# Performance work log

Measured on AMD Instinct MI355X. Metric: run time of the kernel, lower is better.

The kernel has to match this reference:

```python
import jax, jax.numpy as jnp
import numpy as np

B, S, D, H = 2, 2048, 1024, 16
HD = D // H  # 64
ROPE_BASE = 10000.0


def setup_inputs() -> dict:
    key = jax.random.key(0)
    k1, k2, k3 = jax.random.split(key, 3)
    std = 1.0 / np.sqrt(D)
    x = jax.random.normal(k1, (B, S, D), dtype=jnp.float32)
    w_in = jax.random.normal(k2, (3 * D, D), dtype=jnp.float32) * std
    w_out = jax.random.normal(k3, (D, D), dtype=jnp.float32) * (std / np.sqrt(2.0))
    return {"x": x, "w_in": w_in, "w_out": w_out}


def _rope_cos_sin(seq_len, head_dim):
    inv_freq = 1.0 / (ROPE_BASE ** (jnp.arange(0, head_dim, 2, dtype=jnp.float32) / head_dim))
    t = jnp.arange(seq_len, dtype=jnp.float32)
    freqs = jnp.einsum("s,d->sd", t, inv_freq)          # [S, HD/2]
    emb = jnp.concatenate([freqs, freqs], axis=-1)       # [S, HD]
    return jnp.cos(emb)[None, :, None, :], jnp.sin(emb)[None, :, None, :]


def _rotate_half(x):
    x1, x2 = jnp.split(x, 2, axis=-1)
    return jnp.concatenate([-x2, x1], axis=-1)


def _apply_rope(x, cos, sin):
    return x * cos + _rotate_half(x) * sin


def reference(x, w_in, w_out):
    b, s, d = x.shape
    # fused QKV projection (no bias)
    qkv = x @ w_in.T                                      # [B, S, 3D]
    q, k, v = jnp.split(qkv, 3, axis=-1)
    q = q.reshape(b, s, H, HD)
    k = k.reshape(b, s, H, HD)
    v = v.reshape(b, s, H, HD)
    # rotary (offset = 0, no KV cache)
    cos, sin = _rope_cos_sin(s, HD)
    q = _apply_rope(q, cos, sin)
    k = _apply_rope(k, cos, sin)
    # causal SDPA, scale 1/sqrt(head_dim)
    scale = 1.0 / jnp.sqrt(jnp.asarray(HD, dtype=x.dtype))
    scores = jnp.einsum("bqhd,bkhd->bhqk", q, k) * scale  # [B, H, S, S]
    causal = jnp.tril(jnp.ones((s, s), dtype=bool))
    scores = jnp.where(causal, scores, jnp.asarray(-jnp.inf, dtype=scores.dtype))
    attn = jax.nn.softmax(scores, axis=-1)
    out = jnp.einsum("bhqk,bkhd->bqhd", attn, v).reshape(b, s, d)
    return out @ w_out.T
```

## Files before the change

kernel.cpp:

```cpp
#include <hip/hip_runtime.h>
#include <hip/hip_bf16.h>
#include <math.h>

#define NB 2
#define NS 2048
#define ND 1024
#define NH 16
#define HD 64
#define BS (NB*NS)
#define D3 (3*ND)
#define NT (NS/64)

typedef __bf16 bf16;
typedef __bf16 bf16x4 __attribute__((ext_vector_type(4)));
typedef __bf16 bf16x8 __attribute__((ext_vector_type(8)));
typedef float f32x4 __attribute__((ext_vector_type(4)));

#define MFMA16(a,b,c) __builtin_amdgcn_mfma_f32_16x16x32_bf16(a,b,c,0,0,0)

static __device__ inline f32x4 zero4() { f32x4 z; z[0]=0.f; z[1]=0.f; z[2]=0.f; z[3]=0.f; return z; }

__device__ __forceinline__ void gload_lds16(const bf16* g, bf16* l) {
    __builtin_amdgcn_global_load_lds(
        (__attribute__((address_space(1))) unsigned int*)g,
        (__attribute__((address_space(3))) unsigned int*)l, 16, 0, 0);
}

#define CVT1 (BS*ND/8)
#define CVT2 (D3*ND/8)
#define CVT3 (ND*ND/8)
#define CVTN (CVT1+CVT2+CVT3)
__global__ __launch_bounds__(256) void prep(
    const float* __restrict__ x, const float* __restrict__ w_in, const float* __restrict__ w_out,
    bf16* __restrict__ xb, bf16* __restrict__ winb, bf16* __restrict__ woutb,
    float2* __restrict__ csT)
{
    int i = blockIdx.x * 256 + threadIdx.x;
    if (i < CVTN) {
        const float* in; bf16* out; int j;
        if (i < CVT1)            { in = x;     out = xb;    j = i; }
        else if (i < CVT1+CVT2)  { in = w_in;  out = winb;  j = i - CVT1; }
        else                     { in = w_out; out = woutb; j = i - CVT1 - CVT2; }
        const float4* p = (const float4*)in;
        float4 a = p[j*2], b = p[j*2+1];
        bf16x8 o;
        o[0]=(bf16)a.x; o[1]=(bf16)a.y; o[2]=(bf16)a.z; o[3]=(bf16)a.w;
        o[4]=(bf16)b.x; o[5]=(bf16)b.y; o[6]=(bf16)b.z; o[7]=(bf16)b.w;
        ((bf16x8*)out)[j] = o;
    } else {
        int k = i - CVTN;
        int s = k >> 5, j = k & 31;
        float inv = __expf(-(float)j * (9.210340372f * 0.03125f));
        float ang = (float)s * inv;
        csT[k] = make_float2(cosf(ang), sinf(ang));
    }
}

template<int EPI>
__global__ __launch_bounds__(256) void gemm_bt(
    const bf16* __restrict__ A, const bf16* __restrict__ Bm,
    float* __restrict__ C, bf16* __restrict__ Qb, bf16* __restrict__ Kb, bf16* __restrict__ Vt,
    const float2* __restrict__ csT,
    int M, int N, int K)
{
    __shared__ bf16 As[2][128*64];
    __shared__ bf16 Bs[2][128*64];
    int t = threadIdx.x;
    int lane = t & 63, w = t >> 6;
    int wr = w >> 1, wc = w & 1;
    int lr = lane & 15, lg = lane >> 4;
    int m0 = blockIdx.y * 128, n0 = blockIdx.x * 128;

    int srow = lane >> 3;
    int schunk = (lane & 7) ^ srow;
    const bf16* gA = &A [(size_t)(m0 + w*32 + srow)*K + schunk*8];
    const bf16* gB = &Bm[(size_t)(n0 + w*32 + srow)*K + schunk*8];

    auto stage = [&](int kt) {
        int buf = kt & 1;
        bf16* lA = &As[buf][w*2048];
        bf16* lB = &Bs[buf][w*2048];
        int k0 = kt * 64;
        #pragma unroll
        for (int i=0;i<4;i++) {
            gload_lds16(gA + (size_t)(i*8)*K + k0, lA + i*512);
            gload_lds16(gB + (size_t)(i*8)*K + k0, lB + i*512);
        }
    };

    f32x4 acc[4][4];
    for (int m=0;m<4;m++) for (int n=0;n<4;n++) acc[m][n] = zero4();

    int nt = K >> 6;
    stage(0);
    stage(1);

    for (int kt = 0; kt < nt; kt++) {
        int cur = kt & 1;
        if (kt < nt-1) asm volatile("s_waitcnt vmcnt(8)" ::: "memory");
        else           asm volatile("s_waitcnt vmcnt(0)" ::: "memory");
        __builtin_amdgcn_s_barrier();
        __builtin_amdgcn_sched_barrier(0);

        bf16x8 af[2][4], bfr[2][4];
        #pragma unroll
        for (int ks=0;ks<2;ks++) {
            #pragma unroll
            for (int m=0;m<4;m++) {
                int row = wr*64 + m*16 + lr;
                af[ks][m] = *(const bf16x8*)&As[cur][row*64 + (((ks*4+lg) ^ (row&7))*8)];
            }
            #pragma unroll
            for (int n=0;n<4;n++) {
                int row = wc*64 + n*16 + lr;
                bfr[ks][n] = *(const bf16x8*)&Bs[cur][row*64 + (((ks*4+lg) ^ (row&7))*8)];
            }
        }
        asm volatile("s_waitcnt lgkmcnt(0)" ::: "memory");
        __builtin_amdgcn_sched_barrier(0);
        __builtin_amdgcn_s_barrier();
        __builtin_amdgcn_sched_barrier(0);

        if (kt + 2 < nt) stage(kt + 2);

        __builtin_amdgcn_s_setprio(1);
        #pragma unroll
        for (int ks=0;ks<2;ks++)
            #pragma unroll
            for (int m=0;m<4;m++)
                #pragma unroll
                for (int n=0;n<4;n++)
                    acc[m][n] = MFMA16(af[ks][m], bfr[ks][n], acc[m][n]);
        __builtin_amdgcn_s_setprio(0);
    }

    if (EPI == 0) {
        for (int m=0;m<4;m++) for (int n=0;n<4;n++) {
            int grow = m0 + wr*64 + m*16 + lg*4;
            int gcol = n0 + wc*64 + n*16 + lr;
            for (int r=0;r<4;r++)
                C[(size_t)(grow+r) * N + gcol] = acc[m][n][r];
        }
    } else {
        int which = n0 >> 10;
        if (which == 2) {
            for (int m=0;m<4;m++) for (int n=0;n<4;n++) {
                int grow = m0 + wr*64 + m*16 + lg*4;
                int gcol = n0 + wc*64 + n*16 + lr;
                int h = (gcol & 1023) >> 6, d = gcol & 63;
                int b = grow >> 11, s0 = grow & (NS-1);
                int shi = s0 & ~63, j = s0 & 63;
                int kp = ((j>>5)&1)*32 + ((j>>2)&3)*8 + ((j>>4)&1)*4;
                bf16x4 pv;
                for (int r=0;r<4;r++) pv[r] = (bf16)acc[m][n][r];
                *(bf16x4*)&Vt[((size_t)((b*NH + h)*HD + d))*NS + shi + kp] = pv;
            }
        } else {
            const float qs = 0.125f * 1.44269504f;
            bf16* dst = (which == 0) ? Qb : Kb;
            for (int m=0;m<4;m++) {
                int grow = m0 + wr*64 + m*16 + lg*4;
                #pragma unroll
                for (int n=0;n<2;n++) {
                    int gcol = n0 + wc*64 + n*16 + lr;
                    int h = (gcol & 1023) >> 6, j = gcol & 63;
                    #pragma unroll
                    for (int r=0;r<4;r++) {
                        int gm = grow + r;
                        int b = gm >> 11, s = gm & (NS-1);
                        float2 cs = csT[(s<<5)+j];
                        float x1 = acc[m][n][r], x2 = acc[m][n+2][r];
                        float y1 = x1*cs.x - x2*cs.y;
                        float y2 = x2*cs.x + x1*cs.y;
                        if (which == 0) { y1 *= qs; y2 *= qs; }
                        size_t off = ((size_t)((b*NH + h)*NS + s))*HD;
                        dst[off + j]      = (bf16)y1;
                        dst[off + j + 32] = (bf16)y2;
                    }
                }
            }
        }
    }
}

__global__ __launch_bounds__(256, 4) void attn_fwd(
    const bf16* __restrict__ Qb, const bf16* __restrict__ Kb, const bf16* __restrict__ Vp,
    bf16* __restrict__ AO)
{
    __shared__ bf16 Ks[2][64*64];
    __shared__ bf16 Vs[2][64*64];
    int t = threadIdx.x;
    int lane = t & 63, w = t >> 6;
    int lr = lane & 15, lg = lane >> 4;
    int wgid = blockIdx.x;
    int g = wgid >> 5;
    int qt = (g < 8) ? 31 - g : (g < 16) ? g - 8 : (g < 24) ? 39 - g : g - 16;
    int bh = wgid & 31;
    int b = bh >> 4, h = bh & 15;
    size_t base = (size_t)bh * NS * HD;
    int q0 = qt*64 + w*16;

    bf16x8 qf[2];
    #pragma unroll
    for (int c=0;c<2;c++)
        qf[c] = *(const bf16x8*)&Qb[base + (size_t)(q0+lr)*HD + c*32 + lg*8];

    bf16x8 onesf;
    #pragma unroll
    for (int i=0;i<8;i++) onesf[i] = (bf16)1.0f;

    f32x4 o[4];
    f32x4 lacc = zero4();
    #pragma unroll
    for (int n=0;n<4;n++) o[n] = zero4();
    f32x4 minit;
    minit[0] = -12.f; minit[1] = -12.f; minit[2] = -12.f; minit[3] = -12.f;

    int srow = t >> 3;
    int sch  = t & 7;
    int sslot = sch ^ (srow & 7);
    bf16x8 kr[2], vr[2];

    auto load_window = [&](int kv0) {
        #pragma unroll
        for (int i=0;i<2;i++)
            kr[i] = *(const bf16x8*)&Kb[base + (size_t)(kv0 + i*32 + srow)*HD + sch*8];
        #pragma unroll
        for (int i=0;i<2;i++)
            vr[i] = *(const bf16x8*)&Vp[base + (size_t)(i*32 + srow)*NS + kv0 + sch*8];
    };
    auto store_window = [&](int buf) {
        #pragma unroll
        for (int i=0;i<2;i++)
            *(bf16x8*)&Ks[buf][(i*32 + srow)*64 + sslot*8] = kr[i];
        #pragma unroll
        for (int i=0;i<2;i++)
            *(bf16x8*)&Vs[buf][(i*32 + srow)*64 + sslot*8] = vr[i];
    };

    for (int kt = 0; kt <= qt; kt++) {
        if (kt == 0) { load_window(0); store_window(0); __syncthreads(); }
        int cur = kt & 1;
        int kv0 = kt*64;
        bool last = (kt == qt);
        if (!last) load_window(kv0 + 64);

        const bf16* ksb = &Ks[cur][0];
        const bf16* vsb = &Vs[cur][0];

        f32x4 sc[4];
        __builtin_amdgcn_s_setprio(1);
        #pragma unroll
        for (int kb=0;kb<4;kb++) {
            int row = kb*16 + lr;
            bf16x8 k0 = *(const bf16x8*)&ksb[row*64 + ((lg     ^ (row&7))*8)];
            bf16x8 k1 = *(const bf16x8*)&ksb[row*64 + (((4+lg) ^ (row&7))*8)];
            sc[kb] = MFMA16(k0, qf[0], minit);
            sc[kb] = MFMA16(k1, qf[1], sc[kb]);
        }
        __builtin_amdgcn_s_setprio(0);

        if (last) {
            int qi = q0 + lr;
            #pragma unroll
            for (int kb=0;kb<4;kb++)
                #pragma unroll
                for (int rr=0;rr<4;rr++)
                    if (kv0 + kb*16 + lg*4 + rr > qi) sc[kb][rr] = -__builtin_inff();
        }

        bf16x8 pa[2];
        #pragma unroll
        for (int c=0;c<2;c++) {
            bf16x8 v;
            #pragma unroll
            for (int i=0;i<8;i++) v[i] = (bf16)exp2f(sc[c*2 + (i>>2)][i&3]);
            pa[c] = v;
        }

        __builtin_amdgcn_s_setprio(1);
        #pragma unroll
        for (int c=0;c<2;c++) {
            lacc = MFMA16(onesf, pa[c], lacc);
            #pragma unroll
            for (int n=0;n<4;n++) {
                int row = n*16 + lr;
                bf16x8 vf = *(const bf16x8*)&vsb[row*64 + (((c*4+lg) ^ (row&7))*8)];
                o[n] = MFMA16(vf, pa[c], o[n]);
            }
        }
        __builtin_amdgcn_s_setprio(0);

        if (!last) { store_window(cur^1); __syncthreads(); }
    }

    float inv = 1.0f / lacc[0];
    int q = q0 + lr;
    #pragma unroll
    for (int n=0;n<4;n++) {
        bf16x4 ov;
        #pragma unroll
        for (int rr=0;rr<4;rr++) ov[rr] = (bf16)(o[n][rr] * inv);
        *(bf16x4*)&AO[((size_t)(b*NS + q)*NH + h)*HD + n*16 + lg*4] = ov;
    }
}

extern "C" void kernel_launch(void* const* d_in, const int* in_sizes, int n_in,
                              void* d_out, int out_size, void* d_ws, size_t ws_size,
                              hipStream_t stream) {
    const float* x     = (const float*)d_in[0];
    const float* w_in  = (const float*)d_in[1];
    const float* w_out = (const float*)d_in[2];
    float* out = (float*)d_out;

    char* p = (char*)d_ws;
    bf16* xb    = (bf16*)p; p += (size_t)BS*ND*2;
    bf16* winb  = (bf16*)p; p += (size_t)D3*ND*2;
    bf16* woutb = (bf16*)p; p += (size_t)ND*ND*2;
    bf16* Qb    = (bf16*)p; p += (size_t)NB*NH*NS*HD*2;
    bf16* Kb    = (bf16*)p; p += (size_t)NB*NH*NS*HD*2;
    bf16* Vp    = (bf16*)p; p += (size_t)NB*NH*NS*HD*2;
    bf16* AO    = (bf16*)p; p += (size_t)BS*ND*2;
    float2* csT = (float2*)p; p += (size_t)NS*32*8;

    prep<<<(CVTN + NS*32)/256, 256, 0, stream>>>(x, w_in, w_out, xb, winb, woutb, csT);
    gemm_bt<1><<<dim3(D3/128, BS/128), 256, 0, stream>>>(xb, winb, nullptr, Qb, Kb, Vp,
                                                         csT, BS, D3, ND);
    attn_fwd<<<NB*NH*NT, 256, 0, stream>>>(Qb, Kb, Vp, AO);
    gemm_bt<0><<<dim3(ND/128, BS/128), 256, 0, stream>>>(AO, woutb, out, nullptr, nullptr, nullptr,
                                                         nullptr, BS, ND, ND);
}
```

Measured before the change: 98.67 us.

## Pair complementary query tiles per attention block to share K/V loads

Each attention workgroup now handles two query tiles, qa and NT-1-qa, so every block does the same total causal work. The K/V tile staged in LDS and loaded into registers is reused by both tiles, halving K/V traffic per query. The grid shrinks to 512 blocks and launch bounds drop to 2 waves per SIMD to leave room for the doubled accumulators and the K/V fragments held in registers. The risk is lower occupancy and fewer blocks to hide latency.

```diff
diff --git a/kernel.cpp b/kernel.cpp
--- a/kernel.cpp
+++ b/kernel.cpp
@@ -183,7 +183,7 @@
     }
 }
 
-__global__ __launch_bounds__(256, 4) void attn_fwd(
+__global__ __launch_bounds__(256, 2) void attn_fwd(
     const bf16* __restrict__ Qb, const bf16* __restrict__ Kb, const bf16* __restrict__ Vp,
     bf16* __restrict__ AO)
 {
@@ -193,26 +193,28 @@
     int lane = t & 63, w = t >> 6;
     int lr = lane & 15, lg = lane >> 4;
     int wgid = blockIdx.x;
-    int g = wgid >> 5;
-    int qt = (g < 8) ? 31 - g : (g < 16) ? g - 8 : (g < 24) ? 39 - g : g - 16;
     int bh = wgid & 31;
+    int qa = wgid >> 5;
+    int qb = (NT-1) - qa;
     int b = bh >> 4, h = bh & 15;
     size_t base = (size_t)bh * NS * HD;
-    int q0 = qt*64 + w*16;
-
-    bf16x8 qf[2];
+    int q0a = qa*64 + w*16, q0b = qb*64 + w*16;
+
+    bf16x8 qfA[2], qfB[2];
     #pragma unroll
-    for (int c=0;c<2;c++)
-        qf[c] = *(const bf16x8*)&Qb[base + (size_t)(q0+lr)*HD + c*32 + lg*8];
+    for (int c=0;c<2;c++) {
+        qfA[c] = *(const bf16x8*)&Qb[base + (size_t)(q0a+lr)*HD + c*32 + lg*8];
+        qfB[c] = *(const bf16x8*)&Qb[base + (size_t)(q0b+lr)*HD + c*32 + lg*8];
+    }
 
     bf16x8 onesf;
     #pragma unroll
     for (int i=0;i<8;i++) onesf[i] = (bf16)1.0f;
 
-    f32x4 o[4];
-    f32x4 lacc = zero4();
+    f32x4 oA[4], oB[4];
+    f32x4 laccA = zero4(), laccB = zero4();
     #pragma unroll
-    for (int n=0;n<4;n++) o[n] = zero4();
+    for (int n=0;n<4;n++) { oA[n]=zero4(); oB[n]=zero4(); }
     f32x4 minit;
     minit[0] = -12.f; minit[1] = -12.f; minit[2] = -12.f; minit[3] = -12.f;
 
@@ -238,29 +240,17 @@
             *(bf16x8*)&Vs[buf][(i*32 + srow)*64 + sslot*8] = vr[i];
     };
 
-    for (int kt = 0; kt <= qt; kt++) {
-        if (kt == 0) { load_window(0); store_window(0); __syncthreads(); }
-        int cur = kt & 1;
-        int kv0 = kt*64;
-        bool last = (kt == qt);
-        if (!last) load_window(kv0 + 64);
-
-        const bf16* ksb = &Ks[cur][0];
-        const bf16* vsb = &Vs[cur][0];
-
+    auto process = [&](bf16x8 (&kf)[4][2], bf16x8 (&vf)[2][4], bf16x8* qf,
+                       f32x4& lacc, f32x4* o, bool diag, int kv0, int q0) {
         f32x4 sc[4];
         __builtin_amdgcn_s_setprio(1);
         #pragma unroll
         for (int kb=0;kb<4;kb++) {
-            int row = kb*16 + lr;
-            bf16x8 k0 = *(const bf16x8*)&ksb[row*64 + ((lg     ^ (row&7))*8)];
-            bf16x8 k1 = *(const bf16x8*)&ksb[row*64 + (((4+lg) ^ (row&7))*8)];
-            sc[kb] = MFMA16(k0, qf[0], minit);
-            sc[kb] = MFMA16(k1, qf[1], sc[kb]);
+            sc[kb] = MFMA16(kf[kb][0], qf[0], minit);
+            sc[kb] = MFMA16(kf[kb][1], qf[1], sc[kb]);
         }
         __builtin_amdgcn_s_setprio(0);
-
-        if (last) {
+        if (diag) {
             int qi = q0 + lr;
             #pragma unroll
             for (int kb=0;kb<4;kb++)
@@ -268,7 +258,6 @@
                 for (int rr=0;rr<4;rr++)
                     if (kv0 + kb*16 + lg*4 + rr > qi) sc[kb][rr] = -__builtin_inff();
         }
-
         bf16x8 pa[2];
         #pragma unroll
         for (int c=0;c<2;c++) {
@@ -277,31 +266,62 @@
             for (int i=0;i<8;i++) v[i] = (bf16)exp2f(sc[c*2 + (i>>2)][i&3]);
             pa[c] = v;
         }
-
         __builtin_amdgcn_s_setprio(1);
         #pragma unroll
         for (int c=0;c<2;c++) {
             lacc = MFMA16(onesf, pa[c], lacc);
             #pragma unroll
+            for (int n=0;n<4;n++)
+                o[n] = MFMA16(vf[c][n], pa[c], o[n]);
+        }
+        __builtin_amdgcn_s_setprio(0);
+    };
+
+    for (int kt = 0; kt <= qb; kt++) {
+        if (kt == 0) { load_window(0); store_window(0); __syncthreads(); }
+        int cur = kt & 1;
+        int kv0 = kt*64;
+        bool last = (kt == qb);
+        if (!last) load_window(kv0 + 64);
+
+        const bf16* ksb = &Ks[cur][0];
+        const bf16* vsb = &Vs[cur][0];
+
+        bf16x8 kf[4][2], vf[2][4];
+        #pragma unroll
+        for (int kb=0;kb<4;kb++) {
+            int row = kb*16 + lr;
+            kf[kb][0] = *(const bf16x8*)&ksb[row*64 + ((lg     ^ (row&7))*8)];
+            kf[kb][1] = *(const bf16x8*)&ksb[row*64 + (((4+lg) ^ (row&7))*8)];
+        }
+        #pragma unroll
+        for (int c=0;c<2;c++)
+            #pragma unroll
             for (int n=0;n<4;n++) {
                 int row = n*16 + lr;
-                bf16x8 vf = *(const bf16x8*)&vsb[row*64 + (((c*4+lg) ^ (row&7))*8)];
-                o[n] = MFMA16(vf, pa[c], o[n]);
-            }
-        }
-        __builtin_amdgcn_s_setprio(0);
+                vf[c][n] = *(const bf16x8*)&vsb[row*64 + (((c*4+lg) ^ (row&7))*8)];
+            }
+
+        process(kf, vf, qfB, laccB, oB, last, kv0, q0b);
+        if (kt <= qa)
+            process(kf, vf, qfA, laccA, oA, kt==qa, kv0, q0a);
 
         if (!last) { store_window(cur^1); __syncthreads(); }
     }
 
-    float inv = 1.0f / lacc[0];
-    int q = q0 + lr;
+    float invB = 1.0f / laccB[0];
+    float invA = 1.0f / laccA[0];
+    int qB = q0b + lr, qA = q0a + lr;
     #pragma unroll
     for (int n=0;n<4;n++) {
-        bf16x4 ov;
-        #pragma unroll
-        for (int rr=0;rr<4;rr++) ov[rr] = (bf16)(o[n][rr] * inv);
-        *(bf16x4*)&AO[((size_t)(b*NS + q)*NH + h)*HD + n*16 + lg*4] = ov;
+        bf16x4 o1, o2;
+        #pragma unroll
+        for (int rr=0;rr<4;rr++) {
+            o1[rr] = (bf16)(oB[n][rr] * invB);
+            o2[rr] = (bf16)(oA[n][rr] * invA);
+        }
+        *(bf16x4*)&AO[((size_t)(b*NS + qB)*NH + h)*HD + n*16 + lg*4] = o1;
+        *(bf16x4*)&AO[((size_t)(b*NS + qA)*NH + h)*HD + n*16 + lg*4] = o2;
     }
 }
 
@@ -326,7 +346,7 @@
     prep<<<(CVTN + NS*32)/256, 256, 0, stream>>>(x, w_in, w_out, xb, winb, woutb, csT);
     gemm_bt<1><<<dim3(D3/128, BS/128), 256, 0, stream>>>(xb, winb, nullptr, Qb, Kb, Vp,
                                                          csT, BS, D3, ND);
-    attn_fwd<<<NB*NH*NT, 256, 0, stream>>>(Qb, Kb, Vp, AO);
+    attn_fwd<<<NB*NH*(NT/2), 256, 0, stream>>>(Qb, Kb, Vp, AO);
     gemm_bt<0><<<dim3(ND/128, BS/128), 256, 0, stream>>>(AO, woutb, out, nullptr, nullptr, nullptr,
                                                          nullptr, BS, ND, ND);
 }
```

Measured after the change: 98.68 us. No clear change (+0.0%).

## Process 128 query rows per attention block to reuse K/V tiles

Applied to the files above, without the earlier changes.

Each attention workgroup now handles a 128-row query tile, with each wave computing two 16-row sub-tiles. The K and V fragments are read from LDS once into registers and reused for both sub-tiles, halving the number of blocks and the K/V global and LDS traffic per query row. The causal mask is applied only on the last two KV tiles. In exchange the kernel uses more registers (launch bounds lowered to 2 blocks per CU), there are fewer blocks to balance the causal work, and the diagonal tiles do wasted masked work.

```diff
diff --git a/kernel.cpp b/kernel.cpp
--- a/kernel.cpp
+++ b/kernel.cpp
@@ -183,7 +183,7 @@
     }
 }
 
-__global__ __launch_bounds__(256, 4) void attn_fwd(
+__global__ __launch_bounds__(256, 2) void attn_fwd(
     const bf16* __restrict__ Qb, const bf16* __restrict__ Kb, const bf16* __restrict__ Vp,
     bf16* __restrict__ AO)
 {
@@ -193,26 +193,33 @@
     int lane = t & 63, w = t >> 6;
     int lr = lane & 15, lg = lane >> 4;
     int wgid = blockIdx.x;
+    int bh = wgid & 31;
     int g = wgid >> 5;
-    int qt = (g < 8) ? 31 - g : (g < 16) ? g - 8 : (g < 24) ? 39 - g : g - 16;
-    int bh = wgid & 31;
+    int qt2 = (g < 8) ? (15 - g) : (g - 8);
     int b = bh >> 4, h = bh & 15;
     size_t base = (size_t)bh * NS * HD;
-    int q0 = qt*64 + w*16;
-
-    bf16x8 qf[2];
+    int qbase = qt2*128 + w*32;
+    int nvis = 2*qt2 + 2;
+
+    bf16x8 qf[2][2];
     #pragma unroll
-    for (int c=0;c<2;c++)
-        qf[c] = *(const bf16x8*)&Qb[base + (size_t)(q0+lr)*HD + c*32 + lg*8];
+    for (int u=0;u<2;u++)
+        #pragma unroll
+        for (int c=0;c<2;c++)
+            qf[u][c] = *(const bf16x8*)&Qb[base + (size_t)(qbase + u*16 + lr)*HD + c*32 + lg*8];
 
     bf16x8 onesf;
     #pragma unroll
     for (int i=0;i<8;i++) onesf[i] = (bf16)1.0f;
 
-    f32x4 o[4];
-    f32x4 lacc = zero4();
+    f32x4 o[2][4];
+    f32x4 lacc[2];
     #pragma unroll
-    for (int n=0;n<4;n++) o[n] = zero4();
+    for (int u=0;u<2;u++) {
+        lacc[u] = zero4();
+        #pragma unroll
+        for (int n=0;n<4;n++) o[u][n] = zero4();
+    }
     f32x4 minit;
     minit[0] = -12.f; minit[1] = -12.f; minit[2] = -12.f; minit[3] = -12.f;
 
@@ -238,70 +245,91 @@
             *(bf16x8*)&Vs[buf][(i*32 + srow)*64 + sslot*8] = vr[i];
     };
 
-    for (int kt = 0; kt <= qt; kt++) {
+    for (int kt = 0; kt < nvis; kt++) {
         if (kt == 0) { load_window(0); store_window(0); __syncthreads(); }
         int cur = kt & 1;
         int kv0 = kt*64;
-        bool last = (kt == qt);
+        bool last = (kt + 1 == nvis);
         if (!last) load_window(kv0 + 64);
 
         const bf16* ksb = &Ks[cur][0];
         const bf16* vsb = &Vs[cur][0];
 
-        f32x4 sc[4];
-        __builtin_amdgcn_s_setprio(1);
+        bf16x8 kf[4][2], vf[2][4];
         #pragma unroll
         for (int kb=0;kb<4;kb++) {
             int row = kb*16 + lr;
-            bf16x8 k0 = *(const bf16x8*)&ksb[row*64 + ((lg     ^ (row&7))*8)];
-            bf16x8 k1 = *(const bf16x8*)&ksb[row*64 + (((4+lg) ^ (row&7))*8)];
-            sc[kb] = MFMA16(k0, qf[0], minit);
-            sc[kb] = MFMA16(k1, qf[1], sc[kb]);
-        }
-        __builtin_amdgcn_s_setprio(0);
-
-        if (last) {
-            int qi = q0 + lr;
-            #pragma unroll
-            for (int kb=0;kb<4;kb++)
-                #pragma unroll
-                for (int rr=0;rr<4;rr++)
-                    if (kv0 + kb*16 + lg*4 + rr > qi) sc[kb][rr] = -__builtin_inff();
-        }
-
-        bf16x8 pa[2];
-        #pragma unroll
-        for (int c=0;c<2;c++) {
-            bf16x8 v;
-            #pragma unroll
-            for (int i=0;i<8;i++) v[i] = (bf16)exp2f(sc[c*2 + (i>>2)][i&3]);
-            pa[c] = v;
-        }
-
-        __builtin_amdgcn_s_setprio(1);
-        #pragma unroll
-        for (int c=0;c<2;c++) {
-            lacc = MFMA16(onesf, pa[c], lacc);
+            kf[kb][0] = *(const bf16x8*)&ksb[row*64 + ((lg     ^ (row&7))*8)];
+            kf[kb][1] = *(const bf16x8*)&ksb[row*64 + (((4+lg) ^ (row&7))*8)];
+        }
+        #pragma unroll
+        for (int c=0;c<2;c++)
             #pragma unroll
             for (int n=0;n<4;n++) {
                 int row = n*16 + lr;
-                bf16x8 vf = *(const bf16x8*)&vsb[row*64 + (((c*4+lg) ^ (row&7))*8)];
-                o[n] = MFMA16(vf, pa[c], o[n]);
-            }
-        }
+                vf[c][n] = *(const bf16x8*)&vsb[row*64 + (((c*4+lg) ^ (row&7))*8)];
+            }
+
+        f32x4 sc[2][4];
+        __builtin_amdgcn_s_setprio(1);
+        #pragma unroll
+        for (int u=0;u<2;u++)
+            #pragma unroll
+            for (int kb=0;kb<4;kb++) {
+                sc[u][kb] = MFMA16(kf[kb][0], qf[u][0], minit);
+                sc[u][kb] = MFMA16(kf[kb][1], qf[u][1], sc[u][kb]);
+            }
         __builtin_amdgcn_s_setprio(0);
 
+        if (kt >= 2*qt2) {
+            #pragma unroll
+            for (int u=0;u<2;u++) {
+                int qi = qbase + u*16 + lr;
+                #pragma unroll
+                for (int kb=0;kb<4;kb++)
+                    #pragma unroll
+                    for (int rr=0;rr<4;rr++)
+                        if (kv0 + kb*16 + lg*4 + rr > qi) sc[u][kb][rr] = -__builtin_inff();
+            }
+        }
+
+        bf16x8 pa[2][2];
+        #pragma unroll
+        for (int u=0;u<2;u++)
+            #pragma unroll
+            for (int c=0;c<2;c++) {
+                bf16x8 v;
+                #pragma unroll
+                for (int i=0;i<8;i++) v[i] = (bf16)exp2f(sc[u][c*2 + (i>>2)][i&3]);
+                pa[u][c] = v;
+            }
+
+        __builtin_amdgcn_s_setprio(1);
+        #pragma unroll
+        for (int u=0;u<2;u++)
+            #pragma unroll
+            for (int c=0;c<2;c++) {
+                lacc[u] = MFMA16(onesf, pa[u][c], lacc[u]);
+                #pragma unroll
+                for (int n=0;n<4;n++)
+                    o[u][n] = MFMA16(vf[c][n], pa[u][c], o[u][n]);
+            }
+        __builtin_amdgcn_s_setprio(0);
+
         if (!last) { store_window(cur^1); __syncthreads(); }
     }
 
-    float inv = 1.0f / lacc[0];
-    int q = q0 + lr;
     #pragma unroll
-    for (int n=0;n<4;n++) {
-        bf16x4 ov;
-        #pragma unroll
-        for (int rr=0;rr<4;rr++) ov[rr] = (bf16)(o[n][rr] * inv);
-        *(bf16x4*)&AO[((size_t)(b*NS + q)*NH + h)*HD + n*16 + lg*4] = ov;
+    for (int u=0;u<2;u++) {
+        float inv = 1.0f / lacc[u][0];
+        int q = qbase + u*16 + lr;
+        #pragma unroll
+        for (int n=0;n<4;n++) {
+            bf16x4 ov;
+            #pragma unroll
+            for (int rr=0;rr<4;rr++) ov[rr] = (bf16)(o[u][n][rr] * inv);
+            *(bf16x4*)&AO[((size_t)(b*NS + q)*NH + h)*HD + n*16 + lg*4] = ov;
+        }
     }
 }
 
@@ -326,7 +354,7 @@
     prep<<<(CVTN + NS*32)/256, 256, 0, stream>>>(x, w_in, w_out, xb, winb, woutb, csT);
     gemm_bt<1><<<dim3(D3/128, BS/128), 256, 0, stream>>>(xb, winb, nullptr, Qb, Kb, Vp,
                                                          csT, BS, D3, ND);
-    attn_fwd<<<NB*NH*NT, 256, 0, stream>>>(Qb, Kb, Vp, AO);
+    attn_fwd<<<NB*NH*16, 256, 0, stream>>>(Qb, Kb, Vp, AO);
     gemm_bt<0><<<dim3(ND/128, BS/128), 256, 0, stream>>>(AO, woutb, out, nullptr, nullptr, nullptr,
                                                          nullptr, BS, ND, ND);
 }
```

Result: slower. 101.7 us (+3.1%).

## Stage attention K/V tiles via direct global-to-LDS loads with two-tile prefetch

Applied to the files above, without the earlier changes.

Replaces the register-staged K/V window copy in the attention kernel with global_load_lds direct-to-LDS transfers, prefetching two tiles ahead in a double buffer and synchronising with explicit vmcnt waits and barriers. All K and V fragments for the current tile are pulled from LDS into registers up front, so the buffer can be refilled while the MFMAs run. The aim is to hide global load latency and drop the VGPR round trip for the copy. In exchange it raises register pressure, adds a second barrier per tile, and relies on hand-counted vmcnt values being correct.

```diff
diff --git a/kernel.cpp b/kernel.cpp
--- a/kernel.cpp
+++ b/kernel.cpp
@@ -216,47 +216,63 @@
     f32x4 minit;
     minit[0] = -12.f; minit[1] = -12.f; minit[2] = -12.f; minit[3] = -12.f;
 
-    int srow = t >> 3;
-    int sch  = t & 7;
-    int sslot = sch ^ (srow & 7);
-    bf16x8 kr[2], vr[2];
-
-    auto load_window = [&](int kv0) {
-        #pragma unroll
-        for (int i=0;i<2;i++)
-            kr[i] = *(const bf16x8*)&Kb[base + (size_t)(kv0 + i*32 + srow)*HD + sch*8];
-        #pragma unroll
-        for (int i=0;i<2;i++)
-            vr[i] = *(const bf16x8*)&Vp[base + (size_t)(i*32 + srow)*NS + kv0 + sch*8];
+    int srow8 = lane >> 3;
+    int schunk = (lane & 7) ^ srow8;
+    int srcrow = w*8 + srow8;
+    const bf16* gK = Kb + base + (size_t)srcrow*HD + schunk*8;
+    const bf16* gV = Vp + base + (size_t)srcrow*NS + schunk*8;
+
+    auto stage = [&](int kt) {
+        int buf = kt & 1;
+        int kv0 = kt * 64;
+        #pragma unroll
+        for (int i=0;i<2;i++) {
+            gload_lds16(gK + (size_t)(kv0 + i*32)*HD, &Ks[buf][(i*32 + w*8)*64]);
+            gload_lds16(gV + (size_t)(i*32)*NS + kv0, &Vs[buf][(i*32 + w*8)*64]);
+        }
     };
-    auto store_window = [&](int buf) {
-        #pragma unroll
-        for (int i=0;i<2;i++)
-            *(bf16x8*)&Ks[buf][(i*32 + srow)*64 + sslot*8] = kr[i];
-        #pragma unroll
-        for (int i=0;i<2;i++)
-            *(bf16x8*)&Vs[buf][(i*32 + srow)*64 + sslot*8] = vr[i];
-    };
+
+    stage(0);
+    if (qt > 0) stage(1);
 
     for (int kt = 0; kt <= qt; kt++) {
-        if (kt == 0) { load_window(0); store_window(0); __syncthreads(); }
         int cur = kt & 1;
-        int kv0 = kt*64;
         bool last = (kt == qt);
-        if (!last) load_window(kv0 + 64);
+        if (!last) asm volatile("s_waitcnt vmcnt(4)" ::: "memory");
+        else       asm volatile("s_waitcnt vmcnt(0)" ::: "memory");
+        __builtin_amdgcn_s_barrier();
+        __builtin_amdgcn_sched_barrier(0);
 
         const bf16* ksb = &Ks[cur][0];
         const bf16* vsb = &Vs[cur][0];
 
+        bf16x8 kf[4][2], vf[2][4];
+        #pragma unroll
+        for (int kb=0;kb<4;kb++) {
+            int row = kb*16 + lr;
+            kf[kb][0] = *(const bf16x8*)&ksb[row*64 + ((lg     ^ (row&7))*8)];
+            kf[kb][1] = *(const bf16x8*)&ksb[row*64 + (((4+lg) ^ (row&7))*8)];
+        }
+        #pragma unroll
+        for (int c=0;c<2;c++)
+            #pragma unroll
+            for (int n=0;n<4;n++) {
+                int row = n*16 + lr;
+                vf[c][n] = *(const bf16x8*)&vsb[row*64 + (((c*4+lg) ^ (row&7))*8)];
+            }
+        asm volatile("s_waitcnt lgkmcnt(0)" ::: "memory");
+        __builtin_amdgcn_sched_barrier(0);
+        __builtin_amdgcn_s_barrier();
+        __builtin_amdgcn_sched_barrier(0);
+
+        if (kt + 2 <= qt) stage(kt + 2);
+
         f32x4 sc[4];
         __builtin_amdgcn_s_setprio(1);
         #pragma unroll
         for (int kb=0;kb<4;kb++) {
-            int row = kb*16 + lr;
-            bf16x8 k0 = *(const bf16x8*)&ksb[row*64 + ((lg     ^ (row&7))*8)];
-            bf16x8 k1 = *(const bf16x8*)&ksb[row*64 + (((4+lg) ^ (row&7))*8)];
-            sc[kb] = MFMA16(k0, qf[0], minit);
-            sc[kb] = MFMA16(k1, qf[1], sc[kb]);
+            sc[kb] = MFMA16(kf[kb][0], qf[0], minit);
+            sc[kb] = MFMA16(kf[kb][1], qf[1], sc[kb]);
         }
         __builtin_amdgcn_s_setprio(0);
 
@@ -266,7 +282,7 @@
             for (int kb=0;kb<4;kb++)
                 #pragma unroll
                 for (int rr=0;rr<4;rr++)
-                    if (kv0 + kb*16 + lg*4 + rr > qi) sc[kb][rr] = -__builtin_inff();
+                    if (kt*64 + kb*16 + lg*4 + rr > qi) sc[kb][rr] = -__builtin_inff();
         }
 
         bf16x8 pa[2];
@@ -283,15 +299,10 @@
         for (int c=0;c<2;c++) {
             lacc = MFMA16(onesf, pa[c], lacc);
             #pragma unroll
-            for (int n=0;n<4;n++) {
-                int row = n*16 + lr;
-                bf16x8 vf = *(const bf16x8*)&vsb[row*64 + (((c*4+lg) ^ (row&7))*8)];
-                o[n] = MFMA16(vf, pa[c], o[n]);
-            }
+            for (int n=0;n<4;n++)
+                o[n] = MFMA16(vf[c][n], pa[c], o[n]);
         }
         __builtin_amdgcn_s_setprio(0);
-
-        if (!last) { store_window(cur^1); __syncthreads(); }
     }
 
     float inv = 1.0f / lacc[0];
```

Result: faster. 96.35 us (-2.4%).
